# Optimization experiments

Hardware: AMD Instinct MI355X
Metric: run time of the kernel (lower is better)

Reference implementation:

```python
import jax, jax.numpy as jnp
import numpy as np

N_NODES = 100000
N_EDGES = 3200000
D_FEAT = 128
N_CLASSES = 40


def setup_inputs() -> dict:
    key = jax.random.key(0)
    k1, k2, k3, k4 = jax.random.split(key, 4)
    x = jax.random.normal(k1, (N_NODES, D_FEAT), dtype=jnp.float32)
    edge_index = jax.random.randint(k2, (2, N_EDGES), 0, N_NODES, dtype=jnp.int64)
    # torch.nn.Linear default init ~ U(-1/sqrt(fan_in), 1/sqrt(fan_in)); randn is fine for a numeric baseline
    W = jax.random.normal(k3, (N_CLASSES, D_FEAT), dtype=jnp.float32) * (1.0 / np.sqrt(D_FEAT))
    b = jax.random.normal(k4, (N_CLASSES,), dtype=jnp.float32) * 0.01
    return {"x": x, "edge_index": edge_index, "W": W, "b": b, "K": 2}


def _sgc_forward(x, edge_index, W, b, K):
    N = x.shape[0]
    loop = jnp.arange(N, dtype=edge_index.dtype)
    # Outer add_self_loops in SGC.forward, then gcn_norm inside SGConv adds
    # self-loops AGAIN (PyG default add_self_loops=True) -> two self-loops per node.
    row = jnp.concatenate([edge_index[0], loop, loop])
    col = jnp.concatenate([edge_index[1], loop, loop])
    # gcn_norm: deg over destination (col) with unit edge weights
    deg = jax.ops.segment_sum(jnp.ones_like(row, dtype=x.dtype), col, num_segments=N)
    dinv = jnp.where(deg > 0, deg ** -0.5, 0.0)
    norm = dinv[row] * dinv[col]  # [E+2N]
    for _ in range(K):
        # out[col] += norm * x[row]  (K-hop symmetric-normalized propagation)
        x = jax.ops.segment_sum(norm[:, None] * x[row], col, num_segments=N)
    logits = x @ W.T + b  # [N, C]
    return jax.nn.log_softmax(logits, axis=1)


def reference(x, edge_index, W, b, K):
    return _sgc_forward(x, edge_index, W, b, K)
```

## Files before the change

kernel.cpp:

```cpp
#include <hip/hip_runtime.h>
#include <hip/hip_bf16.h>
#include <math.h>

#define DF 128
#define NC 40
#define GST 40
#define RB 8
#define RSZ 256
#define CHUNK 4096
#define CAP 12288

__device__ __forceinline__ float bf2f(unsigned short h) {
  unsigned int u = ((unsigned int)h) << 16;
  union { unsigned int u; float f; } c; c.u = u; return c.f;
}
__device__ __forceinline__ unsigned short f2bf(float x) {
  union { float f; unsigned int u; } c; c.f = x;
  unsigned int u = c.u;
  return (unsigned short)((u + 0x7fffu + ((u >> 16) & 1u)) >> 16);
}
__device__ __forceinline__ float blo(unsigned int u) {
  union { unsigned int u; float f; } c; c.u = u << 16; return c.f;
}
__device__ __forceinline__ float bhi(unsigned int u) {
  union { unsigned int u; float f; } c; c.u = u & 0xffff0000u; return c.f;
}

__global__ __launch_bounds__(512) void k_binB(
    const int* __restrict__ row, const int* __restrict__ col,
    int* __restrict__ cnt, unsigned int* __restrict__ slab, int E, int NB) {
  __shared__ int colS[CHUNK];
  __shared__ int hist[512];
  __shared__ int cursor[512];
  int t = threadIdx.x;
  if (t < NB) hist[t] = 0;
  int s = blockIdx.x * CHUNK, e = min(E, s + CHUNK), n = e - s;
  for (int i = t; i < n; i += 512) colS[i] = col[s + i];
  __syncthreads();
  for (int i = t; i < n; i += 512) atomicAdd(&hist[colS[i] >> RB], 1);
  __syncthreads();
  if (t < NB) cursor[t] = hist[t] ? atomicAdd(&cnt[t], hist[t]) : 0;
  __syncthreads();
  for (int i = t; i < n; i += 512) {
    int c = colS[i];
    int b = c >> RB;
    int p = atomicAdd(&cursor[b], 1);
    slab[(size_t)b * CAP + p] = ((unsigned int)row[s + i] << RB) | (unsigned int)(c & (RSZ - 1));
  }
}

__global__ __launch_bounds__(512) void k_binC(
    const unsigned int* __restrict__ slab, const int* __restrict__ cnt,
    int* __restrict__ off, int* __restrict__ eidx, float* __restrict__ dinv,
    int N, int NB, int E) {
  __shared__ int redS[512];
  __shared__ int hist[RSZ];
  __shared__ int sc[RSZ];
  __shared__ int cur[RSZ];
  int b = blockIdx.x;
  int t = threadIdx.x;
  redS[t] = (t < NB && t < b) ? cnt[t] : 0;
  if (t < RSZ) hist[t] = 0;
  __syncthreads();
  for (int o = 256; o > 0; o >>= 1) {
    if (t < o) redS[t] += redS[t + o];
    __syncthreads();
  }
  int cb = redS[0];
  int cnt_b = cnt[b];
  if (b == 0 && t == 0) off[N] = E;
  const unsigned int* src = slab + (size_t)b * CAP;
  for (int i = t; i < cnt_b; i += 512) atomicAdd(&hist[src[i] & (RSZ - 1)], 1);
  __syncthreads();
  int v = (t < RSZ) ? hist[t] : 0;
  if (t < RSZ) sc[t] = v;
  __syncthreads();
  for (int o = 1; o < RSZ; o <<= 1) {
    int u = (t < RSZ && t >= o) ? sc[t - o] : 0;
    __syncthreads();
    if (t < RSZ) sc[t] += u;
    __syncthreads();
  }
  if (t < RSZ) {
    int pos = cb + sc[t] - v;
    int node = (b << RB) + t;
    if (node < N) {
      off[node] = pos;
      dinv[node] = rsqrtf((float)v + 2.0f);
    }
    cur[t] = pos;
  }
  __syncthreads();
  for (int i = t; i < cnt_b; i += 512) {
    unsigned int en = src[i];
    int p = atomicAdd(&cur[en & (RSZ - 1)], 1);
    eidx[p] = (int)((en >> RB) * (GST * 2u));
  }
}

__global__ __launch_bounds__(128) void k_xw_scale(
    const float* __restrict__ x, const float* __restrict__ W,
    const float* __restrict__ dinv, unsigned short* __restrict__ g0,
    int N, int NH) {
  __shared__ float4 Ws[NC * (DF / 4)];
  for (int i = threadIdx.x; i < NC * (DF / 4); i += blockDim.x)
    Ws[i] = ((const float4*)W)[i];
  __syncthreads();
  int t = blockIdx.x * blockDim.x + threadIdx.x;
  if (t >= NH) return;
  int n0 = t;
  int n1 = t + NH;
  bool has1 = n1 < N;
  int n1c = has1 ? n1 : n0;
  float acc0[NC], acc1[NC];
#pragma unroll
  for (int c = 0; c < NC; ++c) { acc0[c] = 0.f; acc1[c] = 0.f; }
  const float4* xr0 = (const float4*)(x + (size_t)n0 * DF);
  const float4* xr1 = (const float4*)(x + (size_t)n1c * DF);
#pragma unroll 1
  for (int ch = 0; ch < 8; ++ch) {
    float4 a0 = xr0[ch * 4 + 0], a1 = xr0[ch * 4 + 1];
    float4 a2 = xr0[ch * 4 + 2], a3 = xr0[ch * 4 + 3];
    float4 b0 = xr1[ch * 4 + 0], b1 = xr1[ch * 4 + 1];
    float4 b2 = xr1[ch * 4 + 2], b3 = xr1[ch * 4 + 3];
#pragma unroll
    for (int c = 0; c < NC; ++c) {
      float4 w0 = Ws[c * (DF / 4) + ch * 4 + 0];
      float4 w1 = Ws[c * (DF / 4) + ch * 4 + 1];
      float4 w2 = Ws[c * (DF / 4) + ch * 4 + 2];
      float4 w3 = Ws[c * (DF / 4) + ch * 4 + 3];
      acc0[c] += (a0.x * w0.x + a0.y * w0.y + a0.z * w0.z + a0.w * w0.w) +
                 (a1.x * w1.x + a1.y * w1.y + a1.z * w1.z + a1.w * w1.w) +
                 (a2.x * w2.x + a2.y * w2.y + a2.z * w2.z + a2.w * w2.w) +
                 (a3.x * w3.x + a3.y * w3.y + a3.z * w3.z + a3.w * w3.w);
      acc1[c] += (b0.x * w0.x + b0.y * w0.y + b0.z * w0.z + b0.w * w0.w) +
                 (b1.x * w1.x + b1.y * w1.y + b1.z * w1.z + b1.w * w1.w) +
                 (b2.x * w2.x + b2.y * w2.y + b2.z * w2.z + b2.w * w2.w) +
                 (b3.x * w3.x + b3.y * w3.y + b3.z * w3.z + b3.w * w3.w);
    }
  }
  float di0 = dinv[n0];
  unsigned int pk[NC / 2];
#pragma unroll
  for (int c2 = 0; c2 < NC / 2; ++c2) {
    unsigned int lo = f2bf(di0 * acc0[c2 * 2 + 0]);
    unsigned int hi = f2bf(di0 * acc0[c2 * 2 + 1]);
    pk[c2] = lo | (hi << 16);
  }
  uint4* gp0 = (uint4*)(g0 + (size_t)n0 * GST);
#pragma unroll
  for (int q = 0; q < 5; ++q)
    gp0[q] = make_uint4(pk[q * 4 + 0], pk[q * 4 + 1], pk[q * 4 + 2], pk[q * 4 + 3]);
  if (has1) {
    float di1 = dinv[n1];
#pragma unroll
    for (int c2 = 0; c2 < NC / 2; ++c2) {
      unsigned int lo = f2bf(di1 * acc1[c2 * 2 + 0]);
      unsigned int hi = f2bf(di1 * acc1[c2 * 2 + 1]);
      pk[c2] = lo | (hi << 16);
    }
    uint4* gp1 = (uint4*)(g0 + (size_t)n1 * GST);
#pragma unroll
    for (int q = 0; q < 5; ++q)
      gp1[q] = make_uint4(pk[q * 4 + 0], pk[q * 4 + 1], pk[q * 4 + 2], pk[q * 4 + 3]);
  }
}

#define EDGE3U(Q0, Q1, Q2)                                                \
  {                                                                       \
    int sel_ = (slot == 0) ? (Q0) : (slot == 1) ? (Q1) : (Q2);            \
    unsigned v_ = *(const unsigned*)(base + (unsigned)(sel_ + clsoff));   \
    accL += blo(v_); accH += bhi(v_);                                     \
  }
#define EDGE3M(Q0, Q1, Q2, PB)                                            \
  {                                                                       \
    int sel_ = (slot == 0) ? (Q0) : (slot == 1) ? (Q1) : (Q2);            \
    unsigned v_ = *(const unsigned*)(base + (unsigned)(sel_ + clsoff));   \
    float m_ = (sact && (PB) + slot < e) ? 1.f : 0.f;                     \
    accL += m_ * blo(v_); accH += m_ * bhi(v_);                           \
  }

template<int FINAL>
__global__ __launch_bounds__(256) void k_hop(
    const int* __restrict__ off, const int* __restrict__ eidx,
    const float* __restrict__ dinv, const unsigned short* __restrict__ gin,
    unsigned short* __restrict__ gout, const float* __restrict__ bias,
    float* __restrict__ out, int N) {
  int wv = threadIdx.x >> 6;
  int lane = threadIdx.x & 63;
  int node = blockIdx.x * 4 + wv;
  if (node >= N) return;
  int slot = lane / 20;
  int cls = lane - slot * 20;
  bool sact = slot < 3;
  int s = __builtin_amdgcn_readfirstlane(off[node]);
  int e = __builtin_amdgcn_readfirstlane(off[node + 1]);
  float di = dinv[node];
  const char* base = (const char*)gin;
  int clsoff = cls * 4;
  float accL, accH;
  {
    unsigned int v = *(const unsigned int*)(base + (size_t)node * (GST * 2) + clsoff);
    bool s0 = (slot == 0);
    accL = s0 ? 2.f * blo(v) : 0.f;
    accH = s0 ? 2.f * bhi(v) : 0.f;
  }
  int i = s;
  for (; i + 24 <= e; i += 24) {
    int b0  = eidx[i + 0],  b1  = eidx[i + 1],  b2  = eidx[i + 2];
    int b3  = eidx[i + 3],  b4  = eidx[i + 4],  b5  = eidx[i + 5];
    int b6  = eidx[i + 6],  b7  = eidx[i + 7],  b8  = eidx[i + 8];
    int b9  = eidx[i + 9],  b10 = eidx[i + 10], b11 = eidx[i + 11];
    int b12 = eidx[i + 12], b13 = eidx[i + 13], b14 = eidx[i + 14];
    int b15 = eidx[i + 15], b16 = eidx[i + 16], b17 = eidx[i + 17];
    int b18 = eidx[i + 18], b19 = eidx[i + 19], b20 = eidx[i + 20];
    int b21 = eidx[i + 21], b22 = eidx[i + 22], b23 = eidx[i + 23];
    EDGE3U(b0, b1, b2)    EDGE3U(b3, b4, b5)
    EDGE3U(b6, b7, b8)    EDGE3U(b9, b10, b11)
    EDGE3U(b12, b13, b14) EDGE3U(b15, b16, b17)
    EDGE3U(b18, b19, b20) EDGE3U(b21, b22, b23)
  }
  if (i < e) {
    int last = e - 1;
    int q0  = eidx[min(i + 0,  last)], q1  = eidx[min(i + 1,  last)], q2  = eidx[min(i + 2,  last)];
    int q3  = eidx[min(i + 3,  last)], q4  = eidx[min(i + 4,  last)], q5  = eidx[min(i + 5,  last)];
    int q6  = eidx[min(i + 6,  last)], q7  = eidx[min(i + 7,  last)], q8  = eidx[min(i + 8,  last)];
    int q9  = eidx[min(i + 9,  last)], q10 = eidx[min(i + 10, last)], q11 = eidx[min(i + 11, last)];
    int q12 = eidx[min(i + 12, last)], q13 = eidx[min(i + 13, last)], q14 = eidx[min(i + 14, last)];
    int q15 = eidx[min(i + 15, last)], q16 = eidx[min(i + 16, last)], q17 = eidx[min(i + 17, last)];
    int q18 = eidx[min(i + 18, last)], q19 = eidx[min(i + 19, last)], q20 = eidx[min(i + 20, last)];
    int q21 = eidx[min(i + 21, last)], q22 = eidx[min(i + 22, last)], q23 = eidx[min(i + 23, last)];
    EDGE3M(q0, q1, q2, i + 0)     EDGE3M(q3, q4, q5, i + 3)
    EDGE3M(q6, q7, q8, i + 6)     EDGE3M(q9, q10, q11, i + 9)
    EDGE3M(q12, q13, q14, i + 12) EDGE3M(q15, q16, q17, i + 15)
    EDGE3M(q18, q19, q20, i + 18) EDGE3M(q21, q22, q23, i + 21)
  }
  float bL = __shfl(accL, (lane + 20) & 63, 64);
  float cL = __shfl(accL, (lane + 40) & 63, 64);
  float bH = __shfl(accH, (lane + 20) & 63, 64);
  float cH = __shfl(accH, (lane + 40) & 63, 64);
  accL = accL + bL + cL;
  accH = accH + bH + cH;
  bool act20 = (slot == 0);
  if (FINAL) {
    float2 bb = act20 ? *(const float2*)(bias + 2 * cls) : make_float2(0.f, 0.f);
    float v0 = di * accL + bb.x;
    float v1 = di * accH + bb.y;
    float m = act20 ? fmaxf(v0, v1) : -3.0e38f;
#pragma unroll
    for (int o = 32; o > 0; o >>= 1) m = fmaxf(m, __shfl_xor(m, o, 64));
    float ex = act20 ? (expf(v0 - m) + expf(v1 - m)) : 0.f;
    float ssum = ex;
#pragma unroll
    for (int o = 32; o > 0; o >>= 1) ssum += __shfl_xor(ssum, o, 64);
    float lse = m + logf(ssum);
    if (act20) {
      float2 r = make_float2(v0 - lse, v1 - lse);
      *(float2*)(out + (size_t)node * NC + 2 * cls) = r;
    }
  } else {
    if (act20) {
      float sc = di * di;
      unsigned int pk = (unsigned int)f2bf(sc * accL) |
                        ((unsigned int)f2bf(sc * accH) << 16);
      *(unsigned int*)((char*)gout + (size_t)node * (GST * 2) + clsoff) = pk;
    }
  }
}

extern "C" void kernel_launch(void* const* d_in, const int* in_sizes, int n_in,
                              void* d_out, int out_size, void* d_ws, size_t ws_size,
                              hipStream_t stream) {
  const float* x = (const float*)d_in[0];
  const int* ei  = (const int*)d_in[1];
  const float* W = (const float*)d_in[2];
  const float* b = (const float*)d_in[3];
  float* out = (float*)d_out;

  const int N = in_sizes[0] / DF;
  const int E = in_sizes[1] / 2;
  const int NB = (N + RSZ - 1) >> RB;
  const int* row  = ei;
  const int* colv = ei + E;

  char* basep = (char*)d_ws;
  auto alloc = [&](size_t bytes) {
    char* p = basep;
    basep += (bytes + 511) & ~(size_t)511;
    return p;
  };
  int*   cnt    = (int*)  alloc(((size_t)NB) * 4);
  unsigned int* slab = (unsigned int*)alloc((size_t)NB * CAP * 4);
  int*   off    = (int*)  alloc(((size_t)N + 1) * 4);
  int*   eidx   = (int*)  alloc((size_t)E * 4);
  float* dinv   = (float*)alloc((size_t)N * 4);
  unsigned short* g0 = (unsigned short*)alloc((size_t)N * GST * 2);
  unsigned short* g1 = (unsigned short*)alloc((size_t)N * GST * 2);

  const int gBin = (E + CHUNK - 1) / CHUNK;

  hipMemsetAsync(cnt, 0, (size_t)NB * 4, stream);
  k_binB<<<gBin, 512, 0, stream>>>(row, colv, cnt, slab, E, NB);
  k_binC<<<NB, 512, 0, stream>>>(slab, cnt, off, eidx, dinv, N, NB, E);

  const int NH = (N + 1) / 2;
  k_xw_scale<<<(NH + 127) / 128, 128, 0, stream>>>(x, W, dinv, g0, N, NH);

  const int gHop = (N + 3) / 4;
  k_hop<0><<<gHop, 256, 0, stream>>>(off, eidx, dinv, g0, g1, nullptr, nullptr, N);
  k_hop<1><<<gHop, 256, 0, stream>>>(off, eidx, dinv, g1, nullptr, b, out, N);
}
```

Measured before the change: 322.4 us.

## Replace two-pass bucketed CSR build with global-atomic degree count, scan, and fill

Replaces the slab-based two-level binning (per-chunk shared histograms into bucket slabs, then per-bucket local sort) with a classic CSR build: global atomic degree counting, a three-kernel prefix scan, and a fill pass using global atomic cursors with nontemporal stores. This removes the intermediate slab write and read traffic. In exchange it relies on millions of global atomics and scattered writes, and the order of edges within each node becomes nondeterministic. It also launches more kernels and reads the column array twice. k_scan2 runs a single 64-thread wavefront, so it only handles up to 64 scan blocks.

```diff
diff --git a/kernel.cpp b/kernel.cpp
--- a/kernel.cpp
+++ b/kernel.cpp
@@ -5,10 +5,8 @@
 #define DF 128
 #define NC 40
 #define GST 40
-#define RB 8
-#define RSZ 256
-#define CHUNK 4096
-#define CAP 12288
+#define SCB 512
+#define SCE 2048
 
 __device__ __forceinline__ float bf2f(unsigned short h) {
   unsigned int u = ((unsigned int)h) << 16;
@@ -26,75 +24,100 @@
   union { unsigned int u; float f; } c; c.u = u & 0xffff0000u; return c.f;
 }
 
-__global__ __launch_bounds__(512) void k_binB(
-    const int* __restrict__ row, const int* __restrict__ col,
-    int* __restrict__ cnt, unsigned int* __restrict__ slab, int E, int NB) {
-  __shared__ int colS[CHUNK];
-  __shared__ int hist[512];
-  __shared__ int cursor[512];
+__global__ __launch_bounds__(256) void k_deg(
+    const int* __restrict__ col, int* __restrict__ deg, int E) {
+  int i = blockIdx.x * blockDim.x + threadIdx.x;
+  int stride = gridDim.x * blockDim.x;
+  int E4 = E >> 2;
+  const int4* c4 = (const int4*)col;
+  for (int k = i; k < E4; k += stride) {
+    int4 c = c4[k];
+    atomicAdd(&deg[c.x], 1); atomicAdd(&deg[c.y], 1);
+    atomicAdd(&deg[c.z], 1); atomicAdd(&deg[c.w], 1);
+  }
+  for (int k = (E4 << 2) + i; k < E; k += stride) atomicAdd(&deg[col[k]], 1);
+}
+
+__global__ __launch_bounds__(SCB) void k_scan1(
+    const int* __restrict__ deg, int* __restrict__ bsum) {
+  __shared__ int s[SCB];
   int t = threadIdx.x;
-  if (t < NB) hist[t] = 0;
-  int s = blockIdx.x * CHUNK, e = min(E, s + CHUNK), n = e - s;
-  for (int i = t; i < n; i += 512) colS[i] = col[s + i];
-  __syncthreads();
-  for (int i = t; i < n; i += 512) atomicAdd(&hist[colS[i] >> RB], 1);
-  __syncthreads();
-  if (t < NB) cursor[t] = hist[t] ? atomicAdd(&cnt[t], hist[t]) : 0;
-  __syncthreads();
-  for (int i = t; i < n; i += 512) {
-    int c = colS[i];
-    int b = c >> RB;
-    int p = atomicAdd(&cursor[b], 1);
-    slab[(size_t)b * CAP + p] = ((unsigned int)row[s + i] << RB) | (unsigned int)(c & (RSZ - 1));
-  }
-}
-
-__global__ __launch_bounds__(512) void k_binC(
-    const unsigned int* __restrict__ slab, const int* __restrict__ cnt,
-    int* __restrict__ off, int* __restrict__ eidx, float* __restrict__ dinv,
-    int N, int NB, int E) {
-  __shared__ int redS[512];
-  __shared__ int hist[RSZ];
-  __shared__ int sc[RSZ];
-  __shared__ int cur[RSZ];
-  int b = blockIdx.x;
-  int t = threadIdx.x;
-  redS[t] = (t < NB && t < b) ? cnt[t] : 0;
-  if (t < RSZ) hist[t] = 0;
+  const int4* d4 = (const int4*)(deg + (size_t)blockIdx.x * SCE);
+  int4 v = d4[t];
+  s[t] = v.x + v.y + v.z + v.w;
   __syncthreads();
   for (int o = 256; o > 0; o >>= 1) {
-    if (t < o) redS[t] += redS[t + o];
+    if (t < o) s[t] += s[t + o];
     __syncthreads();
   }
-  int cb = redS[0];
-  int cnt_b = cnt[b];
-  if (b == 0 && t == 0) off[N] = E;
-  const unsigned int* src = slab + (size_t)b * CAP;
-  for (int i = t; i < cnt_b; i += 512) atomicAdd(&hist[src[i] & (RSZ - 1)], 1);
+  if (t == 0) bsum[blockIdx.x] = s[0];
+}
+
+__global__ void k_scan2(const int* __restrict__ bsum, int* __restrict__ bbase, int nb) {
+  int t = threadIdx.x;
+  int v0 = (t < nb) ? bsum[t] : 0;
+  int v = v0;
+  for (int o = 1; o < 64; o <<= 1) {
+    int u = __shfl_up(v, o, 64);
+    if (t >= o) v += u;
+  }
+  if (t < nb) bbase[t] = v - v0;
+}
+
+__global__ __launch_bounds__(SCB) void k_scan3(
+    const int* __restrict__ deg, const int* __restrict__ bbase,
+    int* __restrict__ off, int* __restrict__ cur, float* __restrict__ dinv,
+    int N, int E) {
+  __shared__ int s[SCB];
+  int t = threadIdx.x;
+  int base = blockIdx.x * SCE;
+  const int4* d4 = (const int4*)(deg + base);
+  int4 v = d4[t];
+  int sv = v.x + v.y + v.z + v.w;
+  s[t] = sv;
   __syncthreads();
-  int v = (t < RSZ) ? hist[t] : 0;
-  if (t < RSZ) sc[t] = v;
-  __syncthreads();
-  for (int o = 1; o < RSZ; o <<= 1) {
-    int u = (t < RSZ && t >= o) ? sc[t - o] : 0;
+  for (int o = 1; o < SCB; o <<= 1) {
+    int u = (t >= o) ? s[t - o] : 0;
     __syncthreads();
-    if (t < RSZ) sc[t] += u;
+    s[t] += u;
     __syncthreads();
   }
-  if (t < RSZ) {
-    int pos = cb + sc[t] - v;
-    int node = (b << RB) + t;
-    if (node < N) {
-      off[node] = pos;
-      dinv[node] = rsqrtf((float)v + 2.0f);
-    }
-    cur[t] = pos;
-  }
-  __syncthreads();
-  for (int i = t; i < cnt_b; i += 512) {
-    unsigned int en = src[i];
-    int p = atomicAdd(&cur[en & (RSZ - 1)], 1);
-    eidx[p] = (int)((en >> RB) * (GST * 2u));
+  int tb = bbase[blockIdx.x] + s[t] - sv;
+  int i0 = base + t * 4;
+  int p0 = tb;
+  int p1 = p0 + v.x;
+  int p2 = p1 + v.y;
+  int p3 = p2 + v.z;
+  if (i0 + 0 < N) { off[i0+0]=p0; cur[i0+0]=p0; dinv[i0+0]=rsqrtf((float)v.x+2.f); }
+  if (i0 + 1 < N) { off[i0+1]=p1; cur[i0+1]=p1; dinv[i0+1]=rsqrtf((float)v.y+2.f); }
+  if (i0 + 2 < N) { off[i0+2]=p2; cur[i0+2]=p2; dinv[i0+2]=rsqrtf((float)v.z+2.f); }
+  if (i0 + 3 < N) { off[i0+3]=p3; cur[i0+3]=p3; dinv[i0+3]=rsqrtf((float)v.w+2.f); }
+  if (blockIdx.x == 0 && t == 0) off[N] = E;
+}
+
+__global__ __launch_bounds__(256) void k_fill(
+    const int* __restrict__ row, const int* __restrict__ col,
+    int* __restrict__ cur, int* __restrict__ eidx, int E) {
+  int i = blockIdx.x * blockDim.x + threadIdx.x;
+  int stride = gridDim.x * blockDim.x;
+  int E4 = E >> 2;
+  const int4* c4 = (const int4*)col;
+  const int4* r4 = (const int4*)row;
+  for (int k = i; k < E4; k += stride) {
+    int4 c = c4[k];
+    int4 r = r4[k];
+    int p0 = atomicAdd(&cur[c.x], 1);
+    int p1 = atomicAdd(&cur[c.y], 1);
+    int p2 = atomicAdd(&cur[c.z], 1);
+    int p3 = atomicAdd(&cur[c.w], 1);
+    __builtin_nontemporal_store(r.x * (GST * 2), eidx + p0);
+    __builtin_nontemporal_store(r.y * (GST * 2), eidx + p1);
+    __builtin_nontemporal_store(r.z * (GST * 2), eidx + p2);
+    __builtin_nontemporal_store(r.w * (GST * 2), eidx + p3);
+  }
+  for (int k = (E4 << 2) + i; k < E; k += stride) {
+    int p = atomicAdd(&cur[col[k]], 1);
+    __builtin_nontemporal_store(row[k] * (GST * 2), eidx + p);
   }
 }
 
@@ -279,9 +302,11 @@
 
   const int N = in_sizes[0] / DF;
   const int E = in_sizes[1] / 2;
-  const int NB = (N + RSZ - 1) >> RB;
   const int* row  = ei;
   const int* colv = ei + E;
+
+  const int NBLK = (N + SCE - 1) / SCE;
+  const int Npad = NBLK * SCE;
 
   char* basep = (char*)d_ws;
   auto alloc = [&](size_t bytes) {
@@ -289,19 +314,22 @@
     basep += (bytes + 511) & ~(size_t)511;
     return p;
   };
-  int*   cnt    = (int*)  alloc(((size_t)NB) * 4);
-  unsigned int* slab = (unsigned int*)alloc((size_t)NB * CAP * 4);
+  int*   deg    = (int*)  alloc((size_t)Npad * 4);
+  int*   bsum   = (int*)  alloc((size_t)NBLK * 4);
+  int*   bbase  = (int*)  alloc((size_t)NBLK * 4);
   int*   off    = (int*)  alloc(((size_t)N + 1) * 4);
+  int*   cur    = (int*)  alloc((size_t)N * 4);
   int*   eidx   = (int*)  alloc((size_t)E * 4);
   float* dinv   = (float*)alloc((size_t)N * 4);
   unsigned short* g0 = (unsigned short*)alloc((size_t)N * GST * 2);
   unsigned short* g1 = (unsigned short*)alloc((size_t)N * GST * 2);
 
-  const int gBin = (E + CHUNK - 1) / CHUNK;
-
-  hipMemsetAsync(cnt, 0, (size_t)NB * 4, stream);
-  k_binB<<<gBin, 512, 0, stream>>>(row, colv, cnt, slab, E, NB);
-  k_binC<<<NB, 512, 0, stream>>>(slab, cnt, off, eidx, dinv, N, NB, E);
+  hipMemsetAsync(deg, 0, (size_t)Npad * 4, stream);
+  k_deg  <<<1024, 256, 0, stream>>>(colv, deg, E);
+  k_scan1<<<NBLK, SCB, 0, stream>>>(deg, bsum);
+  k_scan2<<<1, 64, 0, stream>>>(bsum, bbase, NBLK);
+  k_scan3<<<NBLK, SCB, 0, stream>>>(deg, bbase, off, cur, dinv, N, E);
+  k_fill <<<1024, 256, 0, stream>>>(row, colv, cur, eidx, E);
 
   const int NH = (N + 1) / 2;
   k_xw_scale<<<(NH + 127) / 128, 128, 0, stream>>>(x, W, dinv, g0, N, NH);
```

Measured after the change: 653.1 us. 103% more time.
